# Kernel tuning notes

Hardware: AMD Instinct MI355X
Metric: run time of the kernel (lower is better)

## Reference

```python
import jax, jax.numpy as jnp
import numpy as np

HEADS = 4
OUT_DIM = 64
NEG_SLOPE = 0.2


def setup_inputs() -> dict:
    key = jax.random.key(0)
    k1, k2, k3, k4 = jax.random.split(key, 4)
    n, in_dim = 4096, 256
    x = jax.random.normal(k1, (n, in_dim), dtype=jnp.float32)
    adj = jax.random.randint(k2, (n, n), 0, 2, dtype=jnp.int32)
    # lin: in_dim -> heads*out_dim (no bias), stored as [in_dim, heads*out_dim]
    W = jax.random.normal(k3, (in_dim, HEADS * OUT_DIM), dtype=jnp.float32) * 0.05
    # att_weight: [heads, 2*out_dim]
    att = jax.random.normal(k4, (HEADS, 2 * OUT_DIM), dtype=jnp.float32) * 0.05
    return {"x": x, "adj": adj, "W": W, "att": att}


def reference(x, adj, W, att):
    n = x.shape[0]
    h = (x @ W).reshape(n, HEADS, OUT_DIM)  # [n, H, D]
    # scores[i,j,h] = att[h] . cat(h_i, h_j) = <h_i, a_src[h]> + <h_j, a_dst[h]>
    a_src, a_dst = att[:, :OUT_DIM], att[:, OUT_DIM:]
    e_src = jnp.einsum('nhd,hd->nh', h, a_src)  # [n, H]
    e_dst = jnp.einsum('nhd,hd->nh', h, a_dst)  # [n, H]
    scores = e_src[:, None, :] + e_dst[None, :, :]  # [n, n, H]
    scores = jax.nn.leaky_relu(scores, negative_slope=NEG_SLOPE)
    mask = (adj > 0)[:, :, None]  # [n, n, 1]
    scores = jnp.where(mask, scores, -jnp.inf)
    alpha = jax.nn.softmax(scores, axis=1)  # softmax over neighbors j
    # h_prime[i,h,d] = sum_j alpha[i,j,h] * h[j,h,d]
    h_prime = jnp.einsum('ijh,jhd->ihd', alpha, h)
    return h_prime.reshape(n, HEADS * OUT_DIM)
```

## Files before the change

### kernel.cpp

```cpp
#include <hip/hip_runtime.h>
#include <hip/hip_bf16.h>

#define HEADS 4
#define ODIM 64
#define HD 256
#define NEG_SLOPE 0.2f
#define SPLITS 8
#define MI 256

typedef __attribute__((ext_vector_type(8))) short bf16x8;
typedef __attribute__((ext_vector_type(4))) float floatx4;
typedef __attribute__((ext_vector_type(2))) float floatx2;

__global__ __launch_bounds__(256) void pack_xw(const float* __restrict__ x,
                                               const float* __restrict__ W,
                                               __hip_bfloat16* __restrict__ xh,
                                               __hip_bfloat16* __restrict__ xl,
                                               __hip_bfloat16* __restrict__ wh,
                                               __hip_bfloat16* __restrict__ wl,
                                               int K, int nxb) {
    const int b = blockIdx.x;
    const int Kc = K >> 5;
    if (b < nxb) {
        const int g = b * 256 + threadIdx.x;
        const int lane = g & 63, frag = g >> 6;
        const int kc = frag % Kc, mc = frag / Kc;
        const int l16 = lane & 15, q = lane >> 4;
        const float* src = x + (size_t)(mc * 16 + l16) * K + kc * 32 + q * 8;
        const float4 v0 = *(const float4*)src;
        const float4 v1 = *(const float4*)(src + 4);
        const float vv[8] = {v0.x, v0.y, v0.z, v0.w, v1.x, v1.y, v1.z, v1.w};
        union { __hip_bfloat16 b[8]; bf16x8 v; } H, L;
        #pragma unroll
        for (int p = 0; p < 8; ++p) {
            H.b[p] = __float2bfloat16(vv[p]);
            L.b[p] = __float2bfloat16(vv[p] - __bfloat162float(H.b[p]));
        }
        *(bf16x8*)&xh[(size_t)frag * 512 + lane * 8] = H.v;
        *(bf16x8*)&xl[(size_t)frag * 512 + lane * 8] = L.v;
    } else {
        const int g = (b - nxb) * 256 + threadIdx.x;
        const int lane = g & 63, frag = g >> 6;
        const int kc = frag % Kc, nc = frag / Kc;
        const int l16 = lane & 15, q = lane >> 4;
        union { __hip_bfloat16 b[8]; bf16x8 v; } H, L;
        #pragma unroll
        for (int p = 0; p < 8; ++p) {
            const float w = W[(size_t)(kc * 32 + q * 8 + p) * HD + nc * 16 + l16];
            H.b[p] = __float2bfloat16(w);
            L.b[p] = __float2bfloat16(w - __bfloat162float(H.b[p]));
        }
        *(bf16x8*)&wh[(size_t)frag * 512 + lane * 8] = H.v;
        *(bf16x8*)&wl[(size_t)frag * 512 + lane * 8] = L.v;
    }
}

__global__ __launch_bounds__(256) void compress_adj(const int* __restrict__ adj,
                                                    unsigned int* __restrict__ bits, int n) {
    const int wave = threadIdx.x >> 6, lane = threadIdx.x & 63;
    const int i = blockIdx.y;
    const int j0 = blockIdx.x * 1024 + wave * 256;
    unsigned long long m[4];
    #pragma unroll
    for (int k = 0; k < 4; ++k)
        m[k] = __ballot(adj[(size_t)i * n + j0 + k * 64 + lane] > 0);
    if (lane == 0) {
        uint4 u, v;
        u.x = (unsigned)m[0]; u.y = (unsigned)(m[0] >> 32);
        u.z = (unsigned)m[1]; u.w = (unsigned)(m[1] >> 32);
        v.x = (unsigned)m[2]; v.y = (unsigned)(m[2] >> 32);
        v.z = (unsigned)m[3]; v.w = (unsigned)(m[3] >> 32);
        *(uint4*)&bits[(size_t)i * (n >> 5) + (j0 >> 5)] = u;
        *(uint4*)&bits[(size_t)i * (n >> 5) + (j0 >> 5) + 4] = v;
    }
}

__global__ __launch_bounds__(128) void gemm_fused(
    const __hip_bfloat16* __restrict__ xh, const __hip_bfloat16* __restrict__ xl,
    const __hip_bfloat16* __restrict__ wh, const __hip_bfloat16* __restrict__ wl,
    const float* __restrict__ att, float2* __restrict__ esrc, float2* __restrict__ edst,
    __hip_bfloat16* __restrict__ hbB, int n, int K) {

    __shared__ __hip_bfloat16 T[64][40];

    const int tid = threadIdx.x, wave = tid >> 6, lane = tid & 63;
    const int q = lane >> 4, l16 = lane & 15;
    const int m0 = blockIdx.x * 32;
    const int head = blockIdx.y;
    const int Kc = K >> 5;
    const int mc = (m0 >> 4) + wave;

    floatx4 acc[4] = {{0.f,0.f,0.f,0.f},{0.f,0.f,0.f,0.f},{0.f,0.f,0.f,0.f},{0.f,0.f,0.f,0.f}};

    const __hip_bfloat16* Axh = xh + (size_t)mc * Kc * 512 + lane * 8;
    const __hip_bfloat16* Axl = xl + (size_t)mc * Kc * 512 + lane * 8;
    const __hip_bfloat16* Bwh = wh + lane * 8;
    const __hip_bfloat16* Bwl = wl + lane * 8;
    #pragma unroll 2
    for (int kc = 0; kc < Kc; ++kc) {
        const bf16x8 ah = *(const bf16x8*)(Axh + (size_t)kc * 512);
        const bf16x8 al = *(const bf16x8*)(Axl + (size_t)kc * 512);
        bf16x8 bh[4], bl[4];
        #pragma unroll
        for (int nt = 0; nt < 4; ++nt) {
            const size_t fo = (size_t)((head * 4 + nt) * Kc + kc) * 512;
            bh[nt] = *(const bf16x8*)(Bwh + fo);
            bl[nt] = *(const bf16x8*)(Bwl + fo);
        }
        #pragma unroll
        for (int nt = 0; nt < 4; ++nt)
            acc[nt] = __builtin_amdgcn_mfma_f32_16x16x32_bf16(ah, bh[nt], acc[nt], 0, 0, 0);
        #pragma unroll
        for (int nt = 0; nt < 4; ++nt)
            acc[nt] = __builtin_amdgcn_mfma_f32_16x16x32_bf16(ah, bl[nt], acc[nt], 0, 0, 0);
        #pragma unroll
        for (int nt = 0; nt < 4; ++nt)
            acc[nt] = __builtin_amdgcn_mfma_f32_16x16x32_bf16(al, bh[nt], acc[nt], 0, 0, 0);
    }

    float as_v[4], ad_v[4];
    #pragma unroll
    for (int nt = 0; nt < 4; ++nt) {
        as_v[nt] = att[head * 2 * ODIM + nt * 16 + l16];
        ad_v[nt] = att[head * 2 * ODIM + ODIM + nt * 16 + l16];
    }
    #pragma unroll
    for (int r = 0; r < 4; ++r) {
        float ps = 0.f, pd = 0.f;
        #pragma unroll
        for (int nt = 0; nt < 4; ++nt) {
            ps = fmaf(acc[nt][r], as_v[nt], ps);
            pd = fmaf(acc[nt][r], ad_v[nt], pd);
        }
        #pragma unroll
        for (int m = 1; m <= 8; m <<= 1) {
            ps += __shfl_xor(ps, m, 64);
            pd += __shfl_xor(pd, m, 64);
        }
        if (l16 == 0) {
            const int i = m0 + wave * 16 + q * 4 + r;
            esrc[head * n + i] = make_float2(__expf(ps), __expf(NEG_SLOPE * ps));
            edst[head * n + i] = make_float2(__expf(pd), __expf(NEG_SLOPE * pd));
        }
    }

    #pragma unroll
    for (int nt = 0; nt < 4; ++nt) {
        union { __hip_bfloat16 b[4]; uint2 u; } pk;
        #pragma unroll
        for (int r = 0; r < 4; ++r) pk.b[r] = __float2bfloat16(acc[nt][r]);
        *(uint2*)&T[nt * 16 + l16][wave * 16 + q * 4] = pk.u;
    }
    __syncthreads();

    #pragma unroll
    for (int ffi = 0; ffi < 2; ++ffi) {
        const int f = wave + ffi * 2;
        const bf16x8 v = *(const bf16x8*)&T[f * 16 + l16][q * 8];
        const size_t frag = ((size_t)head * (n >> 5) + (m0 >> 5)) * 4 + f;
        *(bf16x8*)&hbB[frag * 512 + lane * 8] = v;
    }
}

__global__ __launch_bounds__(256, 2) void aggregate(
    const unsigned int* __restrict__ bits, const float2* __restrict__ esrc,
    const float2* __restrict__ edst, const __hip_bfloat16* __restrict__ hbB,
    float* __restrict__ outsp, float* __restrict__ densp, int n, int KR) {

    __shared__ unsigned int bitsL[MI][17];
    __shared__ float2 edL[512];
    __shared__ __hip_bfloat16 hbL[2][8][512];

    const int tid = threadIdx.x;
    const int wave = tid >> 6, lane = tid & 63;
    const int q = lane >> 4, l16 = lane & 15;
    const int i0 = blockIdx.x * MI;
    const int head = blockIdx.y;
    const int K0 = blockIdx.z * KR;
    const int nw = n >> 5;

    {
        const int dw = tid & 15, rb = tid >> 4;
        #pragma unroll
        for (int rr = 0; rr < 16; ++rr) {
            const int row = rr * 16 + rb;
            bitsL[row][dw] = bits[(size_t)(i0 + row) * nw + (K0 >> 5) + dw];
        }
    }
    for (int t = tid; t < KR; t += 256)
        edL[t] = edst[(size_t)head * n + K0 + t];

    floatx2 es12[4];
    #pragma unroll
    for (int mt = 0; mt < 4; ++mt) {
        const float2 e = esrc[head * n + i0 + wave * 64 + mt * 16 + l16];
        es12[mt][0] = e.x; es12[mt][1] = e.y;
    }

    union { short s[8]; bf16x8 v; } bones;
    #pragma unroll
    for (int p = 0; p < 8; ++p) bones.s[p] = (l16 == 0) ? (short)0x3F80 : (short)0;

    floatx4 acc[4][4];
    floatx4 accd[4];
    #pragma unroll
    for (int mt = 0; mt < 4; ++mt) {
        accd[mt] = (floatx4){0.f, 0.f, 0.f, 0.f};
        #pragma unroll
        for (int nt = 0; nt < 4; ++nt) acc[mt][nt] = (floatx4){0.f, 0.f, 0.f, 0.f};
    }

    const __hip_bfloat16* hbsrc = hbB + ((size_t)head * (n >> 5) + (K0 >> 5)) * 4 * 512;

    uint4 stg0, stg1;
    auto loadChunk = [&](int c) {
        const uint4* src = (const uint4*)(hbsrc + (size_t)c * 4096);
        stg0 = src[tid * 2];
        stg1 = src[tid * 2 + 1];
    };
    auto writeChunk = [&](int buf) {
        uint4* dst = (uint4*)&hbL[buf][0][0];
        dst[tid * 2] = stg0;
        dst[tid * 2 + 1] = stg1;
    };

    auto computeStep = [&](int buf, int sIn, int s) {
        unsigned int bm[4];
        #pragma unroll
        for (int mt = 0; mt < 4; ++mt)
            bm[mt] = (bitsL[wave * 64 + mt * 16 + l16][s] >> (q * 8)) & 0xFFu;
        const float4* ep = (const float4*)&edL[s * 32 + q * 8];
        const float4 e01 = ep[0], e23 = ep[1], e45 = ep[2], e67 = ep[3];
        floatx2 ed[8];
        ed[0][0]=e01.x; ed[0][1]=e01.y;  ed[1][0]=e01.z; ed[1][1]=e01.w;
        ed[2][0]=e23.x; ed[2][1]=e23.y;  ed[3][0]=e23.z; ed[3][1]=e23.w;
        ed[4][0]=e45.x; ed[4][1]=e45.y;  ed[5][0]=e45.z; ed[5][1]=e45.w;
        ed[6][0]=e67.x; ed[6][1]=e67.y;  ed[7][0]=e67.z; ed[7][1]=e67.w;
        bf16x8 bfr[4];
        #pragma unroll
        for (int nt = 0; nt < 4; ++nt)
            bfr[nt] = *(const bf16x8*)&hbL[buf][sIn * 4 + nt][lane * 8];
        #pragma unroll
        for (int mt = 0; mt < 4; ++mt) {
            union { unsigned int u[4]; bf16x8 v; } af;
            #pragma unroll
            for (int p = 0; p < 4; ++p) {
                const floatx2 pa = es12[mt] * ed[2 * p];
                const floatx2 pb = es12[mt] * ed[2 * p + 1];
                const float wa = fmaxf(pa[0], pa[1]);
                const float wb = fmaxf(pb[0], pb[1]);
                const unsigned int mm = ((bm[mt] >> (2 * p)) & 1u) * 0xFFFFu
                                      | ((bm[mt] >> (2 * p + 1)) & 1u) * 0xFFFF0000u;
                af.u[p] = __builtin_amdgcn_perm(__float_as_uint(wb), __float_as_uint(wa),
                                                0x07060302u) & mm;
            }
            #pragma unroll
            for (int nt = 0; nt < 4; ++nt)
                acc[mt][nt] = __builtin_amdgcn_mfma_f32_16x16x32_bf16(af.v, bfr[nt], acc[mt][nt], 0, 0, 0);
            accd[mt] = __builtin_amdgcn_mfma_f32_16x16x32_bf16(af.v, bones.v, accd[mt], 0, 0, 0);
        }
    };

    loadChunk(0);
    writeChunk(0);
    __syncthreads();

    const int NCH = KR >> 6;
    int cur = 0;
    for (int c = 0; c < NCH; ++c) {
        if (c + 1 < NCH) loadChunk(c + 1);
        computeStep(cur, 0, c * 2);
        computeStep(cur, 1, c * 2 + 1);
        if (c + 1 < NCH) {
            writeChunk(cur ^ 1);
            __syncthreads();
            cur ^= 1;
        }
    }

    const size_t sOut = (size_t)blockIdx.z * n * HD;
    #pragma unroll
    for (int mt = 0; mt < 4; ++mt)
        #pragma unroll
        for (int nt = 0; nt < 4; ++nt)
            #pragma unroll
            for (int r = 0; r < 4; ++r)
                outsp[sOut + (size_t)(i0 + wave * 64 + mt * 16 + q * 4 + r) * HD
                      + head * ODIM + nt * 16 + l16] = acc[mt][nt][r];
    if (l16 == 0) {
        #pragma unroll
        for (int mt = 0; mt < 4; ++mt)
            #pragma unroll
            for (int r = 0; r < 4; ++r)
                densp[((size_t)blockIdx.z * n + i0 + wave * 64 + mt * 16 + q * 4 + r) * HEADS + head]
                    = accd[mt][r];
    }
}

__global__ __launch_bounds__(256) void normalize(const float* __restrict__ outsp,
                                                 const float* __restrict__ densp,
                                                 float* __restrict__ out, int n, int splits) {
    const int g = blockIdx.x * 256 + threadIdx.x;
    const int i = g >> 6;
    const int c4 = (g & 63) * 4;
    const int head = c4 >> 6;
    float den = 0.f;
    for (int s = 0; s < splits; ++s) den += densp[((size_t)s * n + i) * HEADS + head];
    float4 v = {0.f, 0.f, 0.f, 0.f};
    for (int s = 0; s < splits; ++s) {
        const float4 t = *(const float4*)&outsp[(size_t)s * n * HD + (size_t)i * HD + c4];
        v.x += t.x; v.y += t.y; v.z += t.z; v.w += t.w;
    }
    const float inv = 1.0f / den;
    v.x *= inv; v.y *= inv; v.z *= inv; v.w *= inv;
    *(float4*)&out[(size_t)i * HD + c4] = v;
}

extern "C" void kernel_launch(void* const* d_in, const int* in_sizes, int n_in,
                              void* d_out, int out_size, void* d_ws, size_t ws_size,
                              hipStream_t stream) {
    const float* x   = (const float*)d_in[0];
    const int*   adj = (const int*)d_in[1];
    const float* W   = (const float*)d_in[2];
    const float* att = (const float*)d_in[3];
    float* out = (float*)d_out;

    const int in_dim = in_sizes[2] / HD;
    const int n = in_sizes[0] / in_dim;

    char* ws = (char*)d_ws;
    size_t off = 0;
    auto alloc = [&](size_t bytes) -> void* {
        void* p = ws + off; off += (bytes + 255) & ~(size_t)255; return p;
    };
    __hip_bfloat16* xh = (__hip_bfloat16*)alloc((size_t)n * in_dim * 2);
    __hip_bfloat16* xl = (__hip_bfloat16*)alloc((size_t)n * in_dim * 2);
    __hip_bfloat16* wh = (__hip_bfloat16*)alloc((size_t)in_dim * HD * 2);
    __hip_bfloat16* wl = (__hip_bfloat16*)alloc((size_t)in_dim * HD * 2);
    float2* esrc = (float2*)alloc((size_t)HEADS * n * 8);
    float2* edst = (float2*)alloc((size_t)HEADS * n * 8);
    __hip_bfloat16* hbB = (__hip_bfloat16*)alloc((size_t)n * HD * 2);
    unsigned int* bits = (unsigned int*)alloc((size_t)n * (n / 8));

    const size_t outB = (size_t)n * HD * 4, denB = (size_t)n * HEADS * 4;
    float* densp = (float*)alloc((size_t)SPLITS * denB);
    float* outsp = (float*)alloc((size_t)SPLITS * outB);

    const int nxb = (n / 16) * (in_dim / 32) * 64 / 256;
    const int nwb = (HD / 16) * (in_dim / 32) * 64 / 256;
    pack_xw<<<nxb + nwb, 256, 0, stream>>>(x, W, xh, xl, wh, wl, in_dim, nxb);
    compress_adj<<<dim3(n / 1024, n), 256, 0, stream>>>(adj, bits, n);
    gemm_fused<<<dim3(n / 32, HEADS), 128, 0, stream>>>(xh, xl, wh, wl, att, esrc, edst, hbB, n, in_dim);
    aggregate<<<dim3(n / MI, HEADS, SPLITS), 256, 0, stream>>>(bits, esrc, edst, hbB, outsp, densp, n, n / SPLITS);
    normalize<<<n * 64 / 256, 256, 0, stream>>>(outsp, densp, out, n, SPLITS);
}
```

Baseline: 147.9 us.

## Fuse adjacency bit-packing into aggregate and process all heads per block

Removes the separate compress_adj kernel and its bitmask buffer. The aggregate kernel now streams the int32 adjacency tile directly, packs it into a 16-bit mask in shared memory, and covers all four heads in one 512-thread block (two row halves × four heads), so each adjacency tile is read once instead of once per head. Row tile drops to 128, and the double-buffered staging is replaced by a single buffer guarded by two barriers per chunk. This exposes more serialization between the load and compute phases, and puts more register pressure on the loader threads.

```diff
diff --git a/kernel.cpp b/kernel.cpp
--- a/kernel.cpp
+++ b/kernel.cpp
@@ -6,7 +6,7 @@
 #define HD 256
 #define NEG_SLOPE 0.2f
 #define SPLITS 8
-#define MI 256
+#define MI 128
 
 typedef __attribute__((ext_vector_type(8))) short bf16x8;
 typedef __attribute__((ext_vector_type(4))) float floatx4;
@@ -55,26 +55,6 @@
     }
 }
 
-__global__ __launch_bounds__(256) void compress_adj(const int* __restrict__ adj,
-                                                    unsigned int* __restrict__ bits, int n) {
-    const int wave = threadIdx.x >> 6, lane = threadIdx.x & 63;
-    const int i = blockIdx.y;
-    const int j0 = blockIdx.x * 1024 + wave * 256;
-    unsigned long long m[4];
-    #pragma unroll
-    for (int k = 0; k < 4; ++k)
-        m[k] = __ballot(adj[(size_t)i * n + j0 + k * 64 + lane] > 0);
-    if (lane == 0) {
-        uint4 u, v;
-        u.x = (unsigned)m[0]; u.y = (unsigned)(m[0] >> 32);
-        u.z = (unsigned)m[1]; u.w = (unsigned)(m[1] >> 32);
-        v.x = (unsigned)m[2]; v.y = (unsigned)(m[2] >> 32);
-        v.z = (unsigned)m[3]; v.w = (unsigned)(m[3] >> 32);
-        *(uint4*)&bits[(size_t)i * (n >> 5) + (j0 >> 5)] = u;
-        *(uint4*)&bits[(size_t)i * (n >> 5) + (j0 >> 5) + 4] = v;
-    }
-}
-
 __global__ __launch_bounds__(128) void gemm_fused(
     const __hip_bfloat16* __restrict__ xh, const __hip_bfloat16* __restrict__ xl,
     const __hip_bfloat16* __restrict__ wh, const __hip_bfloat16* __restrict__ wl,
@@ -162,38 +142,29 @@
     }
 }
 
-__global__ __launch_bounds__(256, 2) void aggregate(
-    const unsigned int* __restrict__ bits, const float2* __restrict__ esrc,
+__global__ __launch_bounds__(512, 2) void aggregate(
+    const int* __restrict__ adj, const float2* __restrict__ esrc,
     const float2* __restrict__ edst, const __hip_bfloat16* __restrict__ hbB,
     float* __restrict__ outsp, float* __restrict__ densp, int n, int KR) {
 
-    __shared__ unsigned int bitsL[MI][17];
-    __shared__ float2 edL[512];
-    __shared__ __hip_bfloat16 hbL[2][8][512];
+    __shared__ __hip_bfloat16 hbL[HEADS][8][512];
+    __shared__ unsigned short mskL[MI][6];
+    __shared__ float2 edL[HEADS][512];
 
     const int tid = threadIdx.x;
     const int wave = tid >> 6, lane = tid & 63;
+    const int head = wave & 3, half = wave >> 2;
     const int q = lane >> 4, l16 = lane & 15;
     const int i0 = blockIdx.x * MI;
-    const int head = blockIdx.y;
-    const int K0 = blockIdx.z * KR;
-    const int nw = n >> 5;
-
-    {
-        const int dw = tid & 15, rb = tid >> 4;
-        #pragma unroll
-        for (int rr = 0; rr < 16; ++rr) {
-            const int row = rr * 16 + rb;
-            bitsL[row][dw] = bits[(size_t)(i0 + row) * nw + (K0 >> 5) + dw];
-        }
-    }
-    for (int t = tid; t < KR; t += 256)
-        edL[t] = edst[(size_t)head * n + K0 + t];
+    const int K0 = blockIdx.y * KR;
+
+    const int ht = tid >> 7, r128 = tid & 127;
+    const int ra = tid >> 2, seg = tid & 3;
 
     floatx2 es12[4];
     #pragma unroll
     for (int mt = 0; mt < 4; ++mt) {
-        const float2 e = esrc[head * n + i0 + wave * 64 + mt * 16 + l16];
+        const float2 e = esrc[head * n + i0 + half * 64 + mt * 16 + l16];
         es12[mt][0] = e.x; es12[mt][1] = e.y;
     }
 
@@ -210,26 +181,34 @@
         for (int nt = 0; nt < 4; ++nt) acc[mt][nt] = (floatx4){0.f, 0.f, 0.f, 0.f};
     }
 
-    const __hip_bfloat16* hbsrc = hbB + ((size_t)head * (n >> 5) + (K0 >> 5)) * 4 * 512;
-
-    uint4 stg0, stg1;
+    uint4 sA[4];
+    int4  aA[4];
+
     auto loadChunk = [&](int c) {
-        const uint4* src = (const uint4*)(hbsrc + (size_t)c * 4096);
-        stg0 = src[tid * 2];
-        stg1 = src[tid * 2 + 1];
+        const uint4* hs = (const uint4*)(hbB + ((size_t)ht * (n >> 5) + (K0 >> 5) + 2 * c) * 2048);
+        #pragma unroll
+        for (int k = 0; k < 4; ++k) sA[k] = hs[k * 128 + r128];
+        const int* ap = adj + (size_t)(i0 + ra) * n + K0 + c * 64 + seg * 16;
+        #pragma unroll
+        for (int k = 0; k < 4; ++k) aA[k] = *(const int4*)(ap + k * 4);
     };
-    auto writeChunk = [&](int buf) {
-        uint4* dst = (uint4*)&hbL[buf][0][0];
-        dst[tid * 2] = stg0;
-        dst[tid * 2 + 1] = stg1;
+    auto stageWrite = [&]() {
+        uint4* hd = (uint4*)&hbL[ht][0][0];
+        #pragma unroll
+        for (int k = 0; k < 4; ++k) hd[k * 128 + r128] = sA[k];
+        const int* av = (const int*)aA;
+        unsigned int m = 0;
+        #pragma unroll
+        for (int b = 0; b < 16; ++b) m |= (unsigned int)(av[b] > 0) << b;
+        mskL[ra][seg] = (unsigned short)m;
     };
 
-    auto computeStep = [&](int buf, int sIn, int s) {
+    auto computeStep = [&](int sIn, int s) {
         unsigned int bm[4];
         #pragma unroll
         for (int mt = 0; mt < 4; ++mt)
-            bm[mt] = (bitsL[wave * 64 + mt * 16 + l16][s] >> (q * 8)) & 0xFFu;
-        const float4* ep = (const float4*)&edL[s * 32 + q * 8];
+            bm[mt] = (*(const unsigned int*)&mskL[half * 64 + mt * 16 + l16][sIn * 2] >> (q * 8)) & 0xFFu;
+        const float4* ep = (const float4*)&edL[head][s * 32 + q * 8];
         const float4 e01 = ep[0], e23 = ep[1], e45 = ep[2], e67 = ep[3];
         floatx2 ed[8];
         ed[0][0]=e01.x; ed[0][1]=e01.y;  ed[1][0]=e01.z; ed[1][1]=e01.w;
@@ -239,7 +218,7 @@
         bf16x8 bfr[4];
         #pragma unroll
         for (int nt = 0; nt < 4; ++nt)
-            bfr[nt] = *(const bf16x8*)&hbL[buf][sIn * 4 + nt][lane * 8];
+            bfr[nt] = *(const bf16x8*)&hbL[head][sIn * 4 + nt][lane * 8];
         #pragma unroll
         for (int mt = 0; mt < 4; ++mt) {
             union { unsigned int u[4]; bf16x8 v; } af;
@@ -262,37 +241,40 @@
     };
 
     loadChunk(0);
-    writeChunk(0);
+    for (int t = tid; t < HEADS * 512; t += 512) {
+        const int h = t >> 9, j = t & 511;
+        edL[h][j] = edst[(size_t)h * n + K0 + j];
+    }
+    stageWrite();
     __syncthreads();
 
     const int NCH = KR >> 6;
-    int cur = 0;
     for (int c = 0; c < NCH; ++c) {
         if (c + 1 < NCH) loadChunk(c + 1);
-        computeStep(cur, 0, c * 2);
-        computeStep(cur, 1, c * 2 + 1);
+        computeStep(0, c * 2);
+        computeStep(1, c * 2 + 1);
         if (c + 1 < NCH) {
-            writeChunk(cur ^ 1);
             __syncthreads();
-            cur ^= 1;
-        }
-    }
-
-    const size_t sOut = (size_t)blockIdx.z * n * HD;
+            stageWrite();
+            __syncthreads();
+        }
+    }
+
+    const size_t sOut = (size_t)blockIdx.y * n * HD;
     #pragma unroll
     for (int mt = 0; mt < 4; ++mt)
         #pragma unroll
         for (int nt = 0; nt < 4; ++nt)
             #pragma unroll
             for (int r = 0; r < 4; ++r)
-                outsp[sOut + (size_t)(i0 + wave * 64 + mt * 16 + q * 4 + r) * HD
+                outsp[sOut + (size_t)(i0 + half * 64 + mt * 16 + q * 4 + r) * HD
                       + head * ODIM + nt * 16 + l16] = acc[mt][nt][r];
     if (l16 == 0) {
         #pragma unroll
         for (int mt = 0; mt < 4; ++mt)
             #pragma unroll
             for (int r = 0; r < 4; ++r)
-                densp[((size_t)blockIdx.z * n + i0 + wave * 64 + mt * 16 + q * 4 + r) * HEADS + head]
+                densp[((size_t)blockIdx.y * n + i0 + half * 64 + mt * 16 + q * 4 + r) * HEADS + head]
                     = accd[mt][r];
     }
 }
@@ -340,7 +322,6 @@
     float2* esrc = (float2*)alloc((size_t)HEADS * n * 8);
     float2* edst = (float2*)alloc((size_t)HEADS * n * 8);
     __hip_bfloat16* hbB = (__hip_bfloat16*)alloc((size_t)n * HD * 2);
-    unsigned int* bits = (unsigned int*)alloc((size_t)n * (n / 8));
 
     const size_t outB = (size_t)n * HD * 4, denB = (size_t)n * HEADS * 4;
     float* densp = (float*)alloc((size_t)SPLITS * denB);
@@ -349,8 +330,7 @@
     const int nxb = (n / 16) * (in_dim / 32) * 64 / 256;
     const int nwb = (HD / 16) * (in_dim / 32) * 64 / 256;
     pack_xw<<<nxb + nwb, 256, 0, stream>>>(x, W, xh, xl, wh, wl, in_dim, nxb);
-    compress_adj<<<dim3(n / 1024, n), 256, 0, stream>>>(adj, bits, n);
     gemm_fused<<<dim3(n / 32, HEADS), 128, 0, stream>>>(xh, xl, wh, wl, att, esrc, edst, hbB, n, in_dim);
-    aggregate<<<dim3(n / MI, HEADS, SPLITS), 256, 0, stream>>>(bits, esrc, edst, hbB, outsp, densp, n, n / SPLITS);
+    aggregate<<<dim3(n / MI, SPLITS), 512, 0, stream>>>(adj, esrc, edst, hbB, outsp, densp, n, n / SPLITS);
     normalize<<<n * 64 / 256, 256, 0, stream>>>(outsp, densp, out, n, SPLITS);
 }
```

After: 161.2 us. +9.0%, slower.
